# Optimization experiments

Hardware: AMD Instinct MI355X
Metric: run time of the kernel (lower is better)

The kernel has to match this reference:

```python
import jax, jax.numpy as jnp
import numpy as np
import math

D_MODEL = 512
NHEAD = 8
HEAD = D_MODEL // NHEAD


def _pe(length, d):
    pos = np.arange(length)[:, None].astype(np.float32)
    div = np.exp(np.arange(0, d, 2).astype(np.float32) * (-math.log(10000.0) / d))
    pe = np.zeros((length, d), np.float32)
    pe[:, 0::2] = np.sin(pos * div)
    pe[:, 1::2] = np.cos(pos * div)
    return jnp.asarray(pe)


def _ln(x, g, b, eps=1e-5):
    m = x.mean(-1, keepdims=True)
    v = ((x - m) ** 2).mean(-1, keepdims=True)
    return (x - m) / jnp.sqrt(v + eps) * g + b


def _mha(q_in, k_in, v_in, w_in, b_in, w_out, b_out, mask=None):
    d = q_in.shape[-1]
    wq, wk, wv = jnp.split(w_in, 3, axis=0)
    bq, bk, bv = jnp.split(b_in, 3, axis=0)
    B, Sq, _ = q_in.shape
    Sk = k_in.shape[1]
    q = (q_in @ wq.T + bq).reshape(B, Sq, NHEAD, HEAD)
    k = (k_in @ wk.T + bk).reshape(B, Sk, NHEAD, HEAD)
    v = (v_in @ wv.T + bv).reshape(B, Sk, NHEAD, HEAD)
    s = jnp.einsum('bqhd,bkhd->bhqk', q, k) / math.sqrt(HEAD)
    if mask is not None:
        s = s + mask
    a = jax.nn.softmax(s, axis=-1)
    o = jnp.einsum('bhqk,bkhd->bqhd', a, v).reshape(B, Sq, d)
    return o @ w_out.T + b_out


def setup_inputs() -> dict:
    rng = np.random.default_rng(0)
    def r(*s):
        return jnp.asarray(rng.standard_normal(s, dtype=np.float32) * 0.02)
    L, d, ff, di, do = 6, 512, 2048, 64, 64
    B, S, T = 4, 512, 256
    return dict(
        src=jnp.asarray(rng.standard_normal((B, S, di), dtype=np.float32)),
        tgt=jnp.asarray(rng.standard_normal((B, T, do), dtype=np.float32)),
        enc_in_w=r(d, di), enc_in_b=r(d),
        dec_in_w=r(d, do), dec_in_b=r(d),
        out_w=r(do, d), out_b=r(do),
        enc_attn_w=r(L, 3 * d, d), enc_attn_b=r(L, 3 * d),
        enc_out_w=r(L, d, d), enc_out_b=r(L, d),
        enc_ff1_w=r(L, ff, d), enc_ff1_b=r(L, ff),
        enc_ff2_w=r(L, d, ff), enc_ff2_b=r(L, d),
        enc_ln1_g=jnp.ones((L, d)), enc_ln1_b=jnp.zeros((L, d)),
        enc_ln2_g=jnp.ones((L, d)), enc_ln2_b=jnp.zeros((L, d)),
        dec_sa_w=r(L, 3 * d, d), dec_sa_b=r(L, 3 * d),
        dec_sa_out_w=r(L, d, d), dec_sa_out_b=r(L, d),
        dec_ca_w=r(L, 3 * d, d), dec_ca_b=r(L, 3 * d),
        dec_ca_out_w=r(L, d, d), dec_ca_out_b=r(L, d),
        dec_ff1_w=r(L, ff, d), dec_ff1_b=r(L, ff),
        dec_ff2_w=r(L, d, ff), dec_ff2_b=r(L, d),
        dec_ln1_g=jnp.ones((L, d)), dec_ln1_b=jnp.zeros((L, d)),
        dec_ln2_g=jnp.ones((L, d)), dec_ln2_b=jnp.zeros((L, d)),
        dec_ln3_g=jnp.ones((L, d)), dec_ln3_b=jnp.zeros((L, d)),
    )


def reference(src, tgt, enc_in_w, enc_in_b, dec_in_w, dec_in_b, out_w, out_b,
              enc_attn_w, enc_attn_b, enc_out_w, enc_out_b,
              enc_ff1_w, enc_ff1_b, enc_ff2_w, enc_ff2_b,
              enc_ln1_g, enc_ln1_b, enc_ln2_g, enc_ln2_b,
              dec_sa_w, dec_sa_b, dec_sa_out_w, dec_sa_out_b,
              dec_ca_w, dec_ca_b, dec_ca_out_w, dec_ca_out_b,
              dec_ff1_w, dec_ff1_b, dec_ff2_w, dec_ff2_b,
              dec_ln1_g, dec_ln1_b, dec_ln2_g, dec_ln2_b, dec_ln3_g, dec_ln3_b):
    d = D_MODEL
    sq = math.sqrt(d)
    S, T = src.shape[1], tgt.shape[1]
    L = enc_attn_w.shape[0]
    # encoder: 'cosine' pos encoding (dropout disabled / eval)
    x = (src @ enc_in_w.T + enc_in_b) * sq + _pe(S, d)[None]
    for i in range(L):
        a = _mha(x, x, x, enc_attn_w[i], enc_attn_b[i], enc_out_w[i], enc_out_b[i])
        x = _ln(x + a, enc_ln1_g[i], enc_ln1_b[i])
        f = jax.nn.relu(x @ enc_ff1_w[i].T + enc_ff1_b[i]) @ enc_ff2_w[i].T + enc_ff2_b[i]
        x = _ln(x + f, enc_ln2_g[i], enc_ln2_b[i])
    memory = x
    # decoder: teacher-forced prefix loop == single causal-masked pass.
    # NOTE: original adds pe[0] to EVERY step (pos_encoder on a length-1 slice).
    y = (tgt @ dec_in_w.T + dec_in_b) * sq + _pe(1, d)[0]
    mask = jnp.where(jnp.tril(jnp.ones((T, T), bool)), 0.0, -1e9).astype(y.dtype)
    for i in range(L):
        a = _mha(y, y, y, dec_sa_w[i], dec_sa_b[i], dec_sa_out_w[i], dec_sa_out_b[i], mask)
        y = _ln(y + a, dec_ln1_g[i], dec_ln1_b[i])
        c = _mha(y, memory, memory, dec_ca_w[i], dec_ca_b[i], dec_ca_out_w[i], dec_ca_out_b[i])
        y = _ln(y + c, dec_ln2_g[i], dec_ln2_b[i])
        f = jax.nn.relu(y @ dec_ff1_w[i].T + dec_ff1_b[i]) @ dec_ff2_w[i].T + dec_ff2_b[i]
        y = _ln(y + f, dec_ln3_g[i], dec_ln3_b[i])
    return y @ out_w.T + out_b
```

## Files before the change

kernel.cpp:

```cpp
#include <hip/hip_runtime.h>
#include <hip/hip_bf16.h>
#include <math.h>

#define BB 4
#define SEQ 512
#define TGT 256
#define DM 512
#define FFD 2048
#define NH 8
#define HD 64
#define NL 6

typedef unsigned short u16;
typedef __attribute__((ext_vector_type(4))) float f4;
typedef __attribute__((ext_vector_type(4))) unsigned short us4;
typedef __attribute__((ext_vector_type(8))) unsigned short us8;
typedef __attribute__((ext_vector_type(8))) short s8;

__device__ inline u16 f2b(float f) {
    __hip_bfloat16 h = __float2bfloat16(f);
    return *reinterpret_cast<u16*>(&h);
}
__device__ inline float b2f(u16 u) {
    unsigned int x = ((unsigned int)u) << 16;
    float f;
    __builtin_memcpy(&f, &x, 4);
    return f;
}
__device__ inline us4 cvt4(f4 v) {
    us4 u;
    u.x = f2b(v.x); u.y = f2b(v.y); u.z = f2b(v.z); u.w = f2b(v.w);
    return u;
}

struct CastSegs {
    const float* src[24];
    u16* dst[24];
    int cum[25];
    int nseg;
};

__global__ __launch_bounds__(256) void castseg_k(CastSegs cs)
{
    const int g0 = blockIdx.x << 11;
    int s = 0;
    while (g0 >= cs.cum[s + 1]) s++;
    const f4* __restrict__ sp = (const f4*)cs.src[s];
    us4* __restrict__ dp = (us4*)cs.dst[s];
    const int base = g0 - cs.cum[s] + (int)threadIdx.x;

    f4 v[8];
#pragma unroll
    for (int k = 0; k < 8; k++) v[k] = sp[base + (k << 8)];
#pragma unroll
    for (int k = 0; k < 8; k++) dp[base + (k << 8)] = cvt4(v[k]);
}

__global__ void kvbias_k(const float* __restrict__ dec_ca_b, float* __restrict__ out)
{
    int idx = blockIdx.x * blockDim.x + threadIdx.x;
    if (idx >= NL * 2 * DM) return;
    int layer = idx >> 10, j = idx & 1023;
    out[idx] = dec_ca_b[layer * 3 * DM + DM + j];
}

template <int RELU, int OUTF32, int BM, int BN, int PE, int KVMAP>
__global__ __launch_bounds__(256) void mgemm_k(
    const u16* __restrict__ A, const u16* __restrict__ W,
    const float* __restrict__ bias, const u16* __restrict__ resid,
    void* __restrict__ Cv, int M, int N, int K, float alpha)
{
    constexpr int MI = BM / 32;
    constexpr int NJ = BN / 32;
    __shared__ u16 As[2][BM][72];
    __shared__ u16 Bs[2][BN][72];
    const int bm = blockIdx.y * BM, bn = blockIdx.x * BN;
    const int tid = threadIdx.x;
    const int wave = tid >> 6, lane = tid & 63;
    const int wr = (wave >> 1) * (BM / 2), wc = (wave & 1) * (BN / 2);
    const int lm = lane & 15, quad = lane >> 4;
    const int sar = (BM == 64) ? (tid >> 2) : (tid >> 3);
    const int sac = (BM == 64) ? ((tid & 3) * 16) : ((tid & 7) * 8);
    const int sbr = (BN == 64) ? (tid >> 2) : (tid >> 3);
    const int sbc = (BN == 64) ? ((tid & 3) * 16) : ((tid & 7) * 8);

    int brow = bn + sbr;
    if (KVMAP) brow = (brow >> 10) * (3 * DM) + DM + (brow & 1023);

    const u16* Arow = A + (size_t)(bm + sar) * K + sac;
    const u16* Wrow = W + (size_t)brow * K + sbc;

    us8 a0 = *(const us8*)(Arow);
    us8 a1;
    if (BM == 64) a1 = *(const us8*)(Arow + 8);
    us8 b0 = *(const us8*)(Wrow);
    us8 b1;
    if (BN == 64) b1 = *(const us8*)(Wrow + 8);

    f4 acc[MI][NJ];
#pragma unroll
    for (int i = 0; i < MI; i++)
#pragma unroll
        for (int j = 0; j < NJ; j++) acc[i][j] = (f4)(0.f);

    const int nk = K >> 6;
    *(us8*)&As[0][sar][sac] = a0;
    if (BM == 64) *(us8*)&As[0][sar][sac + 8] = a1;
    *(us8*)&Bs[0][sbr][sbc] = b0;
    if (BN == 64) *(us8*)&Bs[0][sbr][sbc + 8] = b1;
    __syncthreads();

    for (int t = 0; t < nk; t++) {
        const int cb = t & 1;
        if (t + 1 < nk) {
            int off = (t + 1) << 6;
            a0 = *(const us8*)(Arow + off);
            if (BM == 64) a1 = *(const us8*)(Arow + off + 8);
            b0 = *(const us8*)(Wrow + off);
            if (BN == 64) b1 = *(const us8*)(Wrow + off + 8);
        }
#pragma unroll
        for (int ks = 0; ks < 2; ks++) {
            s8 af[MI], bfr[NJ];
#pragma unroll
            for (int i = 0; i < MI; i++) af[i] = *(const s8*)&As[cb][wr + i * 16 + lm][ks * 32 + quad * 8];
#pragma unroll
            for (int j = 0; j < NJ; j++) bfr[j] = *(const s8*)&Bs[cb][wc + j * 16 + lm][ks * 32 + quad * 8];
#pragma unroll
            for (int i = 0; i < MI; i++)
#pragma unroll
                for (int j = 0; j < NJ; j++)
                    acc[i][j] = __builtin_amdgcn_mfma_f32_16x16x32_bf16(af[i], bfr[j], acc[i][j], 0, 0, 0);
        }
        if (t + 1 < nk) {
            const int nb = cb ^ 1;
            *(us8*)&As[nb][sar][sac] = a0;
            if (BM == 64) *(us8*)&As[nb][sar][sac + 8] = a1;
            *(us8*)&Bs[nb][sbr][sbc] = b0;
            if (BN == 64) *(us8*)&Bs[nb][sbr][sbc + 8] = b1;
            __syncthreads();
        }
    }

#pragma unroll
    for (int j = 0; j < NJ; j++) {
        int n = bn + wc + j * 16 + lm;
        float bv = bias[n];
        float dv = 0.f;
        if (PE == 1) dv = expf((float)(n & ~1) * (-9.210340371976184f / (float)DM));
#pragma unroll
        for (int i = 0; i < MI; i++) {
#pragma unroll
            for (int r = 0; r < 4; r++) {
                int m = bm + wr + i * 16 + quad * 4 + r;
                float v = (acc[i][j][r] + bv) * alpha;
                if (PE == 1) {
                    float ang = (float)(m & (SEQ - 1)) * dv;
                    v += (n & 1) ? cosf(ang) : sinf(ang);
                }
                if (PE == 2) { if (n & 1) v += 1.f; }
                if (RELU) v = fmaxf(v, 0.f);
                size_t off = (size_t)m * N + n;
                if (resid) v += b2f(resid[off]);
                if (OUTF32) ((float*)Cv)[off] = v;
                else        ((u16*)Cv)[off]  = f2b(v);
            }
        }
    }
}

template <int CAUSAL>
__global__ __launch_bounds__(256) void flash_k(
    const u16* __restrict__ Q, int qs,
    const u16* __restrict__ Kp, int ks,
    const u16* __restrict__ V, int vs,
    u16* __restrict__ O, int Sq, int Sk)
{
    __shared__ u16 Qs[64][72];
    __shared__ u16 Ks[128][72];
    __shared__ u16 Vs[64][136];
    __shared__ u16 Ps[4][16][136];
    const int bm = blockIdx.x * 64;
    const int bh = blockIdx.y, b = bh >> 3, h = bh & 7;
    const int tid = threadIdx.x;
    const int wave = tid >> 6, lane = tid & 63;
    const int lm = lane & 15, quad = lane >> 4;

    const u16* Qb = Q + (size_t)(b * Sq + bm) * qs + h * HD;
    {
        int r = tid >> 2, c = (tid & 3) * 16;
        *(us8*)&Qs[r][c]     = *(const us8*)(Qb + (size_t)r * qs + c);
        *(us8*)&Qs[r][c + 8] = *(const us8*)(Qb + (size_t)r * qs + c + 8);
    }

    float mrow[4], lrow[4];
    f4 o[4];
#pragma unroll
    for (int r = 0; r < 4; r++) { mrow[r] = -1e30f; lrow[r] = 0.f; }
#pragma unroll
    for (int nt = 0; nt < 4; nt++) o[nt] = (f4)(0.f);

    const u16* Kb = Kp + (size_t)(b * Sk) * ks + h * HD;
    const u16* Vb = V + (size_t)(b * Sk) * vs + h * HD;
    int nkt = Sk >> 7;
    if (CAUSAL) { int lim = (bm + 63) / 128 + 1; if (lim < nkt) nkt = lim; }

    const int vd = tid & 63, vkb = tid >> 6;
    const int kr = tid >> 3, kc8 = (tid & 7) * 8;

    for (int kt = 0; kt < nkt; kt++) {
        const u16* Kt = Kb + ((size_t)kt << 7) * ks;
        const u16* Vt = Vb + ((size_t)kt << 7) * vs;
#pragma unroll
        for (int p = 0; p < 4; p++) {
            int r = p * 32 + kr;
            *(us8*)&Ks[r][kc8] = *(const us8*)(Kt + (size_t)r * ks + kc8);
        }
#pragma unroll
        for (int p = 0; p < 32; p++) {
            int kv = p * 4 + vkb;
            Vs[vd][kv] = Vt[(size_t)kv * vs + vd];
        }
        __syncthreads();

        f4 sa[8];
#pragma unroll
        for (int nt = 0; nt < 8; nt++) sa[nt] = (f4)(0.f);
#pragma unroll
        for (int ks2 = 0; ks2 < 2; ks2++) {
            s8 aq = *(const s8*)&Qs[wave * 16 + lm][ks2 * 32 + quad * 8];
#pragma unroll
            for (int nt = 0; nt < 8; nt++) {
                s8 bk = *(const s8*)&Ks[nt * 16 + lm][ks2 * 32 + quad * 8];
                sa[nt] = __builtin_amdgcn_mfma_f32_16x16x32_bf16(aq, bk, sa[nt], 0, 0, 0);
            }
        }
        float tmx[4] = {-1e30f, -1e30f, -1e30f, -1e30f};
#pragma unroll
        for (int nt = 0; nt < 8; nt++) {
#pragma unroll
            for (int r = 0; r < 4; r++) {
                float v = sa[nt][r] * 0.125f;
                if (CAUSAL) {
                    int col = (kt << 7) + nt * 16 + lm;
                    int row = bm + wave * 16 + quad * 4 + r;
                    if (col > row) v = -1e30f;
                }
                sa[nt][r] = v;
                tmx[r] = fmaxf(tmx[r], v);
            }
        }
#pragma unroll
        for (int st = 1; st < 16; st <<= 1)
#pragma unroll
            for (int r = 0; r < 4; r++) tmx[r] = fmaxf(tmx[r], __shfl_xor(tmx[r], st));
        float al[4];
#pragma unroll
        for (int r = 0; r < 4; r++) {
            float mn = fmaxf(mrow[r], tmx[r]);
            al[r] = __expf(mrow[r] - mn);
            mrow[r] = mn;
        }
        float ts[4] = {0.f, 0.f, 0.f, 0.f};
#pragma unroll
        for (int nt = 0; nt < 8; nt++) {
#pragma unroll
            for (int r = 0; r < 4; r++) {
                float pe = __expf(sa[nt][r] - mrow[r]);
                sa[nt][r] = pe;
                ts[r] += pe;
            }
        }
#pragma unroll
        for (int st = 1; st < 16; st <<= 1)
#pragma unroll
            for (int r = 0; r < 4; r++) ts[r] += __shfl_xor(ts[r], st);
#pragma unroll
        for (int r = 0; r < 4; r++) lrow[r] = lrow[r] * al[r] + ts[r];
#pragma unroll
        for (int nt = 0; nt < 4; nt++)
#pragma unroll
            for (int r = 0; r < 4; r++) o[nt][r] *= al[r];
#pragma unroll
        for (int nt = 0; nt < 8; nt++)
#pragma unroll
            for (int r = 0; r < 4; r++)
                Ps[wave][quad * 4 + r][nt * 16 + lm] = f2b(sa[nt][r]);
#pragma unroll
        for (int kc = 0; kc < 4; kc++) {
            s8 ap = *(const s8*)&Ps[wave][lm][kc * 32 + quad * 8];
#pragma unroll
            for (int nt = 0; nt < 4; nt++) {
                s8 bv = *(const s8*)&Vs[nt * 16 + lm][kc * 32 + quad * 8];
                o[nt] = __builtin_amdgcn_mfma_f32_16x16x32_bf16(ap, bv, o[nt], 0, 0, 0);
            }
        }
        __syncthreads();
    }

    float inv[4];
#pragma unroll
    for (int r = 0; r < 4; r++) inv[r] = 1.f / lrow[r];
#pragma unroll
    for (int nt = 0; nt < 4; nt++) {
#pragma unroll
        for (int r = 0; r < 4; r++) {
            int m = bm + wave * 16 + quad * 4 + r;
            O[(size_t)(b * Sq + m) * DM + h * HD + nt * 16 + lm] = f2b(o[nt][r] * inv[r]);
        }
    }
}

__global__ __launch_bounds__(256) void ln_k(u16* __restrict__ x,
                                            const float* __restrict__ g,
                                            const float* __restrict__ b)
{
    const int wave = threadIdx.x >> 6, lane = threadIdx.x & 63;
    const int row = blockIdx.x * 4 + wave;
    u16* xr = x + (size_t)row * DM + lane * 8;
    us8 v8 = *(const us8*)xr;
    float v[8];
    float s = 0.f;
#pragma unroll
    for (int e = 0; e < 8; e++) { v[e] = b2f(v8[e]); s += v[e]; }
#pragma unroll
    for (int st = 1; st < 64; st <<= 1) s += __shfl_xor(s, st);
    float mean = s * (1.f / DM);
    float q = 0.f;
#pragma unroll
    for (int e = 0; e < 8; e++) { float d = v[e] - mean; q += d * d; }
#pragma unroll
    for (int st = 1; st < 64; st <<= 1) q += __shfl_xor(q, st);
    float rstd = rsqrtf(q * (1.f / DM) + 1e-5f);
    f4 g0 = *(const f4*)(g + lane * 8), g1 = *(const f4*)(g + lane * 8 + 4);
    f4 b0 = *(const f4*)(b + lane * 8), b1 = *(const f4*)(b + lane * 8 + 4);
    us8 o;
#pragma unroll
    for (int e = 0; e < 4; e++) {
        o[e]     = f2b((v[e]     - mean) * rstd * g0[e] + b0[e]);
        o[e + 4] = f2b((v[e + 4] - mean) * rstd * g1[e] + b1[e]);
    }
    *(us8*)xr = o;
}

static inline dim3 mg(int M, int N, int BM, int BN) { return dim3(N / BN, M / BM); }

extern "C" void kernel_launch(void* const* d_in, const int* in_sizes, int n_in,
                              void* d_out, int out_size, void* d_ws, size_t ws_size,
                              hipStream_t stream)
{
    const float* src       = (const float*)d_in[0];
    const float* tgt       = (const float*)d_in[1];
    const float* enc_in_w  = (const float*)d_in[2];
    const float* enc_in_b  = (const float*)d_in[3];
    const float* dec_in_w  = (const float*)d_in[4];
    const float* dec_in_b  = (const float*)d_in[5];
    const float* out_w     = (const float*)d_in[6];
    const float* out_b     = (const float*)d_in[7];
    const float* enc_attn_w = (const float*)d_in[8];
    const float* enc_attn_b = (const float*)d_in[9];
    const float* enc_out_w  = (const float*)d_in[10];
    const float* enc_out_b  = (const float*)d_in[11];
    const float* enc_ff1_w  = (const float*)d_in[12];
    const float* enc_ff1_b  = (const float*)d_in[13];
    const float* enc_ff2_w  = (const float*)d_in[14];
    const float* enc_ff2_b  = (const float*)d_in[15];
    const float* enc_ln1_g  = (const float*)d_in[16];
    const float* enc_ln1_b  = (const float*)d_in[17];
    const float* enc_ln2_g  = (const float*)d_in[18];
    const float* enc_ln2_b  = (const float*)d_in[19];
    const float* dec_sa_w     = (const float*)d_in[20];
    const float* dec_sa_b     = (const float*)d_in[21];
    const float* dec_sa_out_w = (const float*)d_in[22];
    const float* dec_sa_out_b = (const float*)d_in[23];
    const float* dec_ca_w     = (const float*)d_in[24];
    const float* dec_ca_b     = (const float*)d_in[25];
    const float* dec_ca_out_w = (const float*)d_in[26];
    const float* dec_ca_out_b = (const float*)d_in[27];
    const float* dec_ff1_w    = (const float*)d_in[28];
    const float* dec_ff1_b    = (const float*)d_in[29];
    const float* dec_ff2_w    = (const float*)d_in[30];
    const float* dec_ff2_b    = (const float*)d_in[31];
    const float* dec_ln1_g    = (const float*)d_in[32];
    const float* dec_ln1_b    = (const float*)d_in[33];
    const float* dec_ln2_g    = (const float*)d_in[34];
    const float* dec_ln2_b    = (const float*)d_in[35];
    const float* dec_ln3_g    = (const float*)d_in[36];
    const float* dec_ln3_b    = (const float*)d_in[37];

    const int ME = BB * SEQ;
    const int MD = BB * TGT;
    const int BH = BB * NH;
    const float SQD = 22.627416997969522f;

    const size_t SZ_ATTN = (size_t)NL * 3 * DM * DM;
    const size_t SZ_OUT  = (size_t)NL * DM * DM;
    const size_t SZ_FF   = (size_t)NL * FFD * DM;

    float* fp = (float*)d_ws;
    float* kvbias = fp; fp += NL * 2 * DM;
    u16* p = (u16*)fp;
    u16* xa   = p; p += (size_t)ME * DM;
    u16* xb   = p; p += (size_t)ME * DM;
    u16* reg1 = p; p += (size_t)ME * FFD;
    u16* tbuf = p; p += (size_t)ME * DM;
    u16* ya   = p; p += (size_t)MD * DM;
    u16* yb   = p; p += (size_t)MD * DM;
    u16* kvall = p; p += (size_t)ME * NL * 2 * DM;
    u16* src_b     = p; p += (size_t)ME * HD;
    u16* tgt_b     = p; p += (size_t)MD * HD;
    u16* enc_in_wb = p; p += (size_t)DM * HD;
    u16* dec_in_wb = p; p += (size_t)DM * HD;
    u16* out_wb    = p; p += (size_t)HD * DM;
    u16* enc_at_wb = p; p += SZ_ATTN;
    u16* enc_ow_wb = p; p += SZ_OUT;
    u16* enc_f1_wb = p; p += SZ_FF;
    u16* enc_f2_wb = p; p += SZ_FF;
    u16* dec_sa_wb = p; p += SZ_ATTN;
    u16* dec_sao_wb = p; p += SZ_OUT;
    u16* dec_ca_wb = p; p += SZ_ATTN;
    u16* dec_cao_wb = p; p += SZ_OUT;
    u16* dec_f1_wb = p; p += SZ_FF;
    u16* dec_f2_wb = p; p += SZ_FF;

    CastSegs cs;
    int ns = 0;
    auto seg = [&](const float* s, u16* d, size_t n) {
        cs.src[ns] = s; cs.dst[ns] = d;
        cs.cum[ns + 1] = cs.cum[ns] + (int)(n / 4);
        ns++;
    };
    cs.cum[0] = 0;
    seg(src,          src_b,     (size_t)ME * HD);
    seg(tgt,          tgt_b,     (size_t)MD * HD);
    seg(enc_in_w,     enc_in_wb, (size_t)DM * HD);
    seg(dec_in_w,     dec_in_wb, (size_t)DM * HD);
    seg(out_w,        out_wb,    (size_t)HD * DM);
    seg(enc_attn_w,   enc_at_wb, SZ_ATTN);
    seg(enc_out_w,    enc_ow_wb, SZ_OUT);
    seg(enc_ff1_w,    enc_f1_wb, SZ_FF);
    seg(enc_ff2_w,    enc_f2_wb, SZ_FF);
    seg(dec_sa_w,     dec_sa_wb, SZ_ATTN);
    seg(dec_sa_out_w, dec_sao_wb, SZ_OUT);
    seg(dec_ca_w,     dec_ca_wb, SZ_ATTN);
    seg(dec_ca_out_w, dec_cao_wb, SZ_OUT);
    seg(dec_ff1_w,    dec_f1_wb, SZ_FF);
    seg(dec_ff2_w,    dec_f2_wb, SZ_FF);
    cs.nseg = ns;
    castseg_k<<<cs.cum[ns] >> 11, 256, 0, stream>>>(cs);
    kvbias_k<<<(NL * 2 * DM + 255) / 256, 256, 0, stream>>>(dec_ca_b, kvbias);

    mgemm_k<0, 0, 64, 32, 1, 0><<<mg(ME, DM, 64, 32), 256, 0, stream>>>(src_b, enc_in_wb, enc_in_b, nullptr, xa, ME, DM, HD, SQD);

    u16* cur = xa; u16* alt = xb;
    for (int i = 0; i < NL; i++) {
        const u16* W = enc_at_wb + (size_t)i * 3 * DM * DM;
        const float* Bw = enc_attn_b + (size_t)i * 3 * DM;
        mgemm_k<0, 0, 64, 64, 0, 0><<<mg(ME, 3 * DM, 64, 64), 256, 0, stream>>>(cur, W, Bw, nullptr, reg1, ME, 3 * DM, DM, 1.f);
        flash_k<0><<<dim3(SEQ / 64, BH), 256, 0, stream>>>(reg1, 3 * DM, reg1 + DM, 3 * DM, reg1 + 2 * DM, 3 * DM, tbuf, SEQ, SEQ);
        mgemm_k<0, 0, 32, 32, 0, 0><<<mg(ME, DM, 32, 32), 256, 0, stream>>>(tbuf, enc_ow_wb + (size_t)i * DM * DM, enc_out_b + (size_t)i * DM, cur, alt, ME, DM, DM, 1.f);
        ln_k<<<ME / 4, 256, 0, stream>>>(alt, enc_ln1_g + (size_t)i * DM, enc_ln1_b + (size_t)i * DM);
        { u16* t = cur; cur = alt; alt = t; }
        mgemm_k<1, 0, 64, 64, 0, 0><<<mg(ME, FFD, 64, 64), 256, 0, stream>>>(cur, enc_f1_wb + (size_t)i * FFD * DM, enc_ff1_b + (size_t)i * FFD, nullptr, reg1, ME, FFD, DM, 1.f);
        mgemm_k<0, 0, 32, 32, 0, 0><<<mg(ME, DM, 32, 32), 256, 0, stream>>>(reg1, enc_f2_wb + (size_t)i * DM * FFD, enc_ff2_b + (size_t)i * DM, cur, alt, ME, DM, FFD, 1.f);
        ln_k<<<ME / 4, 256, 0, stream>>>(alt, enc_ln2_g + (size_t)i * DM, enc_ln2_b + (size_t)i * DM);
        { u16* t = cur; cur = alt; alt = t; }
    }
    u16* mem = cur;

    mgemm_k<0, 0, 64, 64, 0, 1><<<mg(ME, NL * 2 * DM, 64, 64), 256, 0, stream>>>(mem, dec_ca_wb, kvbias, nullptr, kvall, ME, NL * 2 * DM, DM, 1.f);

    mgemm_k<0, 0, 32, 32, 2, 0><<<mg(MD, DM, 32, 32), 256, 0, stream>>>(tgt_b, dec_in_wb, dec_in_b, nullptr, ya, MD, DM, HD, SQD);

    u16* dc = ya; u16* da = yb;
    for (int i = 0; i < NL; i++) {
        const u16* W = dec_sa_wb + (size_t)i * 3 * DM * DM;
        const float* Bw = dec_sa_b + (size_t)i * 3 * DM;
        mgemm_k<0, 0, 64, 32, 0, 0><<<mg(MD, 3 * DM, 64, 32), 256, 0, stream>>>(dc, W, Bw, nullptr, reg1, MD, 3 * DM, DM, 1.f);
        flash_k<1><<<dim3(TGT / 64, BH), 256, 0, stream>>>(reg1, 3 * DM, reg1 + DM, 3 * DM, reg1 + 2 * DM, 3 * DM, tbuf, TGT, TGT);
        mgemm_k<0, 0, 32, 32, 0, 0><<<mg(MD, DM, 32, 32), 256, 0, stream>>>(tbuf, dec_sao_wb + (size_t)i * DM * DM, dec_sa_out_b + (size_t)i * DM, dc, da, MD, DM, DM, 1.f);
        ln_k<<<MD / 4, 256, 0, stream>>>(da, dec_ln1_g + (size_t)i * DM, dec_ln1_b + (size_t)i * DM);
        { u16* t = dc; dc = da; da = t; }

        const u16* Wc = dec_ca_wb + (size_t)i * 3 * DM * DM;
        const float* Bc = dec_ca_b + (size_t)i * 3 * DM;
        u16* qbuf = reg1;
        mgemm_k<0, 0, 32, 32, 0, 0><<<mg(MD, DM, 32, 32), 256, 0, stream>>>(dc, Wc, Bc, nullptr, qbuf, MD, DM, DM, 1.f);
        const u16* kvl = kvall + (size_t)i * 2 * DM;
        flash_k<0><<<dim3(TGT / 64, BH), 256, 0, stream>>>(qbuf, DM, kvl, NL * 2 * DM, kvl + DM, NL * 2 * DM, tbuf, TGT, SEQ);
        mgemm_k<0, 0, 32, 32, 0, 0><<<mg(MD, DM, 32, 32), 256, 0, stream>>>(tbuf, dec_cao_wb + (size_t)i * DM * DM, dec_ca_out_b + (size_t)i * DM, dc, da, MD, DM, DM, 1.f);
        ln_k<<<MD / 4, 256, 0, stream>>>(da, dec_ln2_g + (size_t)i * DM, dec_ln2_b + (size_t)i * DM);
        { u16* t = dc; dc = da; da = t; }

        mgemm_k<1, 0, 64, 32, 0, 0><<<mg(MD, FFD, 64, 32), 256, 0, stream>>>(dc, dec_f1_wb + (size_t)i * FFD * DM, dec_ff1_b + (size_t)i * FFD, nullptr, reg1, MD, FFD, DM, 1.f);
        mgemm_k<0, 0, 32, 32, 0, 0><<<mg(MD, DM, 32, 32), 256, 0, stream>>>(reg1, dec_f2_wb + (size_t)i * DM * FFD, dec_ff2_b + (size_t)i * DM, dc, da, MD, DM, FFD, 1.f);
        ln_k<<<MD / 4, 256, 0, stream>>>(da, dec_ln3_g + (size_t)i * DM, dec_ln3_b + (size_t)i * DM);
        { u16* t = dc; dc = da; da = t; }
    }

    mgemm_k<0, 1, 32, 32, 0, 0><<<mg(MD, HD, 32, 32), 256, 0, stream>>>(dc, out_wb, out_b, nullptr, (float*)d_out, MD, HD, DM, 1.f);
}
```

Baseline: 1.211 ms.

## Fuse LayerNorm into GEMM epilogues and prologues via atomic row statistics

Removes the standalone LayerNorm kernels. GEMMs that produce a residual sum now accumulate per-row sum and sum-of-squares with atomics into a zeroed stats buffer. Consumer GEMMs normalize the A operand while staging it into shared memory and normalize the residual in their epilogue. This cuts 30 kernel launches and their global read/write passes. The cost is extra atomics and per-element normalize math in the GEMMs. Variance computed as E[x²]−mean² in fp32 is less numerically robust than the two-pass version.

```diff
diff --git a/kernel.cpp b/kernel.cpp
--- a/kernel.cpp
+++ b/kernel.cpp
@@ -33,6 +33,21 @@
     return u;
 }
 
+__device__ inline us8 lnx8(us8 y, float mean, float rstd,
+                           const float* __restrict__ g, const float* __restrict__ b) {
+    us8 o;
+#pragma unroll
+    for (int e = 0; e < 8; e++)
+        o[e] = f2b((b2f(y[e]) - mean) * rstd * g[e] + b[e]);
+    return o;
+}
+
+__global__ __launch_bounds__(256) void zero_k(float* __restrict__ p, int n)
+{
+    int i = blockIdx.x * 256 + threadIdx.x;
+    if (i < n) p[i] = 0.f;
+}
+
 struct CastSegs {
     const float* src[24];
     u16* dst[24];
@@ -64,11 +79,15 @@
     out[idx] = dec_ca_b[layer * 3 * DM + DM + j];
 }
 
-template <int RELU, int OUTF32, int BM, int BN, int PE, int KVMAP>
+template <int RELU, int OUTF32, int BM, int BN, int PE, int KVMAP,
+          int LNA, int LNRES, int LNOUT>
 __global__ __launch_bounds__(256) void mgemm_k(
     const u16* __restrict__ A, const u16* __restrict__ W,
     const float* __restrict__ bias, const u16* __restrict__ resid,
-    void* __restrict__ Cv, int M, int N, int K, float alpha)
+    void* __restrict__ Cv,
+    const float* __restrict__ lnst_in, const float* __restrict__ g_in,
+    const float* __restrict__ b_in, float* __restrict__ lnst_out,
+    int M, int N, int K, float alpha)
 {
     constexpr int MI = BM / 32;
     constexpr int NJ = BN / 32;
@@ -90,6 +109,14 @@
     const u16* Arow = A + (size_t)(bm + sar) * K + sac;
     const u16* Wrow = W + (size_t)brow * K + sbc;
 
+    float meanA = 0.f, rstdA = 0.f;
+    if (LNA) {
+        int rowA = bm + sar;
+        float s = lnst_in[rowA * 2], q = lnst_in[rowA * 2 + 1];
+        meanA = s * (1.f / DM);
+        rstdA = rsqrtf(q * (1.f / DM) - meanA * meanA + 1e-5f);
+    }
+
     us8 a0 = *(const us8*)(Arow);
     us8 a1;
     if (BM == 64) a1 = *(const us8*)(Arow + 8);
@@ -104,16 +131,22 @@
         for (int j = 0; j < NJ; j++) acc[i][j] = (f4)(0.f);
 
     const int nk = K >> 6;
-    *(us8*)&As[0][sar][sac] = a0;
-    if (BM == 64) *(us8*)&As[0][sar][sac + 8] = a1;
+    if (LNA) {
+        *(us8*)&As[0][sar][sac] = lnx8(a0, meanA, rstdA, g_in + sac, b_in + sac);
+        if (BM == 64) *(us8*)&As[0][sar][sac + 8] = lnx8(a1, meanA, rstdA, g_in + sac + 8, b_in + sac + 8);
+    } else {
+        *(us8*)&As[0][sar][sac] = a0;
+        if (BM == 64) *(us8*)&As[0][sar][sac + 8] = a1;
+    }
     *(us8*)&Bs[0][sbr][sbc] = b0;
     if (BN == 64) *(us8*)&Bs[0][sbr][sbc + 8] = b1;
     __syncthreads();
 
     for (int t = 0; t < nk; t++) {
         const int cb = t & 1;
+        int off = 0;
         if (t + 1 < nk) {
-            int off = (t + 1) << 6;
+            off = (t + 1) << 6;
             a0 = *(const us8*)(Arow + off);
             if (BM == 64) a1 = *(const us8*)(Arow + off + 8);
             b0 = *(const us8*)(Wrow + off);
@@ -134,18 +167,46 @@
         }
         if (t + 1 < nk) {
             const int nb = cb ^ 1;
-            *(us8*)&As[nb][sar][sac] = a0;
-            if (BM == 64) *(us8*)&As[nb][sar][sac + 8] = a1;
+            if (LNA) {
+                *(us8*)&As[nb][sar][sac] = lnx8(a0, meanA, rstdA, g_in + off + sac, b_in + off + sac);
+                if (BM == 64) *(us8*)&As[nb][sar][sac + 8] = lnx8(a1, meanA, rstdA, g_in + off + sac + 8, b_in + off + sac + 8);
+            } else {
+                *(us8*)&As[nb][sar][sac] = a0;
+                if (BM == 64) *(us8*)&As[nb][sar][sac + 8] = a1;
+            }
             *(us8*)&Bs[nb][sbr][sbc] = b0;
             if (BN == 64) *(us8*)&Bs[nb][sbr][sbc + 8] = b1;
             __syncthreads();
         }
     }
 
+    float meanR[MI][4], rstdR[MI][4];
+    if (LNRES) {
+#pragma unroll
+        for (int i = 0; i < MI; i++)
+#pragma unroll
+            for (int r = 0; r < 4; r++) {
+                int m = bm + wr + i * 16 + quad * 4 + r;
+                float s = lnst_in[m * 2], q = lnst_in[m * 2 + 1];
+                float mn = s * (1.f / DM);
+                meanR[i][r] = mn;
+                rstdR[i][r] = rsqrtf(q * (1.f / DM) - mn * mn + 1e-5f);
+            }
+    }
+    float so[MI][4], qo[MI][4];
+    if (LNOUT) {
+#pragma unroll
+        for (int i = 0; i < MI; i++)
+#pragma unroll
+            for (int r = 0; r < 4; r++) { so[i][r] = 0.f; qo[i][r] = 0.f; }
+    }
+
 #pragma unroll
     for (int j = 0; j < NJ; j++) {
         int n = bn + wc + j * 16 + lm;
         float bv = bias[n];
+        float gR = 0.f, bRv = 0.f;
+        if (LNRES) { gR = g_in[n]; bRv = b_in[n]; }
         float dv = 0.f;
         if (PE == 1) dv = expf((float)(n & ~1) * (-9.210340371976184f / (float)DM));
 #pragma unroll
@@ -161,10 +222,37 @@
                 if (PE == 2) { if (n & 1) v += 1.f; }
                 if (RELU) v = fmaxf(v, 0.f);
                 size_t off = (size_t)m * N + n;
-                if (resid) v += b2f(resid[off]);
+                if (resid) {
+                    float rv = b2f(resid[off]);
+                    if (LNRES) rv = (rv - meanR[i][r]) * rstdR[i][r] * gR + bRv;
+                    v += rv;
+                }
                 if (OUTF32) ((float*)Cv)[off] = v;
                 else        ((u16*)Cv)[off]  = f2b(v);
+                if (LNOUT) { so[i][r] += v; qo[i][r] += v * v; }
             }
+        }
+    }
+
+    if (LNOUT) {
+#pragma unroll
+        for (int st = 1; st < 16; st <<= 1)
+#pragma unroll
+            for (int i = 0; i < MI; i++)
+#pragma unroll
+                for (int r = 0; r < 4; r++) {
+                    so[i][r] += __shfl_xor(so[i][r], st);
+                    qo[i][r] += __shfl_xor(qo[i][r], st);
+                }
+        if (lm == 0) {
+#pragma unroll
+            for (int i = 0; i < MI; i++)
+#pragma unroll
+                for (int r = 0; r < 4; r++) {
+                    int m = bm + wr + i * 16 + quad * 4 + r;
+                    atomicAdd(&lnst_out[m * 2],     so[i][r]);
+                    atomicAdd(&lnst_out[m * 2 + 1], qo[i][r]);
+                }
         }
     }
 }
@@ -309,38 +397,6 @@
             O[(size_t)(b * Sq + m) * DM + h * HD + nt * 16 + lm] = f2b(o[nt][r] * inv[r]);
         }
     }
-}
-
-__global__ __launch_bounds__(256) void ln_k(u16* __restrict__ x,
-                                            const float* __restrict__ g,
-                                            const float* __restrict__ b)
-{
-    const int wave = threadIdx.x >> 6, lane = threadIdx.x & 63;
-    const int row = blockIdx.x * 4 + wave;
-    u16* xr = x + (size_t)row * DM + lane * 8;
-    us8 v8 = *(const us8*)xr;
-    float v[8];
-    float s = 0.f;
-#pragma unroll
-    for (int e = 0; e < 8; e++) { v[e] = b2f(v8[e]); s += v[e]; }
-#pragma unroll
-    for (int st = 1; st < 64; st <<= 1) s += __shfl_xor(s, st);
-    float mean = s * (1.f / DM);
-    float q = 0.f;
-#pragma unroll
-    for (int e = 0; e < 8; e++) { float d = v[e] - mean; q += d * d; }
-#pragma unroll
-    for (int st = 1; st < 64; st <<= 1) q += __shfl_xor(q, st);
-    float rstd = rsqrtf(q * (1.f / DM) + 1e-5f);
-    f4 g0 = *(const f4*)(g + lane * 8), g1 = *(const f4*)(g + lane * 8 + 4);
-    f4 b0 = *(const f4*)(b + lane * 8), b1 = *(const f4*)(b + lane * 8 + 4);
-    us8 o;
-#pragma unroll
-    for (int e = 0; e < 4; e++) {
-        o[e]     = f2b((v[e]     - mean) * rstd * g0[e] + b0[e]);
-        o[e + 4] = f2b((v[e + 4] - mean) * rstd * g1[e] + b1[e]);
-    }
-    *(us8*)xr = o;
 }
 
 static inline dim3 mg(int M, int N, int BM, int BN) { return dim3(N / BN, M / BM); }
@@ -398,6 +454,8 @@
     const size_t SZ_FF   = (size_t)NL * FFD * DM;
 
     float* fp = (float*)d_ws;
+    const int ENC_ST = 12 * 2048 * 2, DEC_ST = 18 * 1024 * 2;
+    float* stats = fp; fp += ENC_ST + DEC_ST;
     float* kvbias = fp; fp += NL * 2 * DM;
     u16* p = (u16*)fp;
     u16* xa   = p; p += (size_t)ME * DM;
@@ -422,6 +480,11 @@
     u16* dec_cao_wb = p; p += SZ_OUT;
     u16* dec_f1_wb = p; p += SZ_FF;
     u16* dec_f2_wb = p; p += SZ_FF;
+
+    auto eSt = [&](int i, int s) { return stats + (size_t)(i * 2 + s) * 2048 * 2; };
+    auto dSt = [&](int i, int s) { return stats + ENC_ST + (size_t)(i * 3 + s) * 1024 * 2; };
+
+    zero_k<<<(ENC_ST + DEC_ST + 255) / 256, 256, 0, stream>>>(stats, ENC_ST + DEC_ST);
 
     CastSegs cs;
     int ns = 0;
@@ -450,53 +513,94 @@
     castseg_k<<<cs.cum[ns] >> 11, 256, 0, stream>>>(cs);
     kvbias_k<<<(NL * 2 * DM + 255) / 256, 256, 0, stream>>>(dec_ca_b, kvbias);
 
-    mgemm_k<0, 0, 64, 32, 1, 0><<<mg(ME, DM, 64, 32), 256, 0, stream>>>(src_b, enc_in_wb, enc_in_b, nullptr, xa, ME, DM, HD, SQD);
+    mgemm_k<0, 0, 64, 32, 1, 0, 0, 0, 0><<<mg(ME, DM, 64, 32), 256, 0, stream>>>(
+        src_b, enc_in_wb, enc_in_b, nullptr, xa, nullptr, nullptr, nullptr, nullptr, ME, DM, HD, SQD);
 
     u16* cur = xa; u16* alt = xb;
     for (int i = 0; i < NL; i++) {
         const u16* W = enc_at_wb + (size_t)i * 3 * DM * DM;
         const float* Bw = enc_attn_b + (size_t)i * 3 * DM;
-        mgemm_k<0, 0, 64, 64, 0, 0><<<mg(ME, 3 * DM, 64, 64), 256, 0, stream>>>(cur, W, Bw, nullptr, reg1, ME, 3 * DM, DM, 1.f);
+        const float* pSt = (i > 0) ? eSt(i - 1, 1) : nullptr;
+        const float* pG  = enc_ln2_g + (size_t)(i - 1) * DM;
+        const float* pB  = enc_ln2_b + (size_t)(i - 1) * DM;
+        if (i == 0)
+            mgemm_k<0, 0, 64, 64, 0, 0, 0, 0, 0><<<mg(ME, 3 * DM, 64, 64), 256, 0, stream>>>(
+                cur, W, Bw, nullptr, reg1, nullptr, nullptr, nullptr, nullptr, ME, 3 * DM, DM, 1.f);
+        else
+            mgemm_k<0, 0, 64, 64, 0, 0, 1, 0, 0><<<mg(ME, 3 * DM, 64, 64), 256, 0, stream>>>(
+                cur, W, Bw, nullptr, reg1, pSt, pG, pB, nullptr, ME, 3 * DM, DM, 1.f);
         flash_k<0><<<dim3(SEQ / 64, BH), 256, 0, stream>>>(reg1, 3 * DM, reg1 + DM, 3 * DM, reg1 + 2 * DM, 3 * DM, tbuf, SEQ, SEQ);
-        mgemm_k<0, 0, 32, 32, 0, 0><<<mg(ME, DM, 32, 32), 256, 0, stream>>>(tbuf, enc_ow_wb + (size_t)i * DM * DM, enc_out_b + (size_t)i * DM, cur, alt, ME, DM, DM, 1.f);
-        ln_k<<<ME / 4, 256, 0, stream>>>(alt, enc_ln1_g + (size_t)i * DM, enc_ln1_b + (size_t)i * DM);
+        if (i == 0)
+            mgemm_k<0, 0, 32, 32, 0, 0, 0, 0, 1><<<mg(ME, DM, 32, 32), 256, 0, stream>>>(
+                tbuf, enc_ow_wb + (size_t)i * DM * DM, enc_out_b + (size_t)i * DM, cur, alt,
+                nullptr, nullptr, nullptr, eSt(i, 0), ME, DM, DM, 1.f);
+        else
+            mgemm_k<0, 0, 32, 32, 0, 0, 0, 1, 1><<<mg(ME, DM, 32, 32), 256, 0, stream>>>(
+                tbuf, enc_ow_wb + (size_t)i * DM * DM, enc_out_b + (size_t)i * DM, cur, alt,
+                pSt, pG, pB, eSt(i, 0), ME, DM, DM, 1.f);
         { u16* t = cur; cur = alt; alt = t; }
-        mgemm_k<1, 0, 64, 64, 0, 0><<<mg(ME, FFD, 64, 64), 256, 0, stream>>>(cur, enc_f1_wb + (size_t)i * FFD * DM, enc_ff1_b + (size_t)i * FFD, nullptr, reg1, ME, FFD, DM, 1.f);
-        mgemm_k<0, 0, 32, 32, 0, 0><<<mg(ME, DM, 32, 32), 256, 0, stream>>>(reg1, enc_f2_wb + (size_t)i * DM * FFD, enc_ff2_b + (size_t)i * DM, cur, alt, ME, DM, FFD, 1.f);
-        ln_k<<<ME / 4, 256, 0, stream>>>(alt, enc_ln2_g + (size_t)i * DM, enc_ln2_b + (size_t)i * DM);
+        mgemm_k<1, 0, 64, 64, 0, 0, 1, 0, 0><<<mg(ME, FFD, 64, 64), 256, 0, stream>>>(
+            cur, enc_f1_wb + (size_t)i * FFD * DM, enc_ff1_b + (size_t)i * FFD, nullptr, reg1,
+            eSt(i, 0), enc_ln1_g + (size_t)i * DM, enc_ln1_b + (size_t)i * DM, nullptr, ME, FFD, DM, 1.f);
+        mgemm_k<0, 0, 32, 32, 0, 0, 0, 1, 1><<<mg(ME, DM, 32, 32), 256, 0, stream>>>(
+            reg1, enc_f2_wb + (size_t)i * DM * FFD, enc_ff2_b + (size_t)i * DM, cur, alt,
+            eSt(i, 0), enc_ln1_g + (size_t)i * DM, enc_ln1_b + (size_t)i * DM, eSt(i, 1), ME, DM, FFD, 1.f);
         { u16* t = cur; cur = alt; alt = t; }
     }
     u16* mem = cur;
 
-    mgemm_k<0, 0, 64, 64, 0, 1><<<mg(ME, NL * 2 * DM, 64, 64), 256, 0, stream>>>(mem, dec_ca_wb, kvbias, nullptr, kvall, ME, NL * 2 * DM, DM, 1.f);
-
-    mgemm_k<0, 0, 32, 32, 2, 0><<<mg(MD, DM, 32, 32), 256, 0, stream>>>(tgt_b, dec_in_wb, dec_in_b, nullptr, ya, MD, DM, HD, SQD);
+    mgemm_k<0, 0, 64, 64, 0, 1, 1, 0, 0><<<mg(ME, NL * 2 * DM, 64, 64), 256, 0, stream>>>(
+        mem, dec_ca_wb, kvbias, nullptr, kvall,
+        eSt(5, 1), enc_ln2_g + (size_t)5 * DM, enc_ln2_b + (size_t)5 * DM, nullptr, ME, NL * 2 * DM, DM, 1.f);
+
+    mgemm_k<0, 0, 32, 32, 2, 0, 0, 0, 0><<<mg(MD, DM, 32, 32), 256, 0, stream>>>(
+        tgt_b, dec_in_wb, dec_in_b, nullptr, ya, nullptr, nullptr, nullptr, nullptr, MD, DM, HD, SQD);
 
     u16* dc = ya; u16* da = yb;
     for (int i = 0; i < NL; i++) {
         const u16* W = dec_sa_wb + (size_t)i * 3 * DM * DM;
         const float* Bw = dec_sa_b + (size_t)i * 3 * DM;
-        mgemm_k<0, 0, 64, 32, 0, 0><<<mg(MD, 3 * DM, 64, 32), 256, 0, stream>>>(dc, W, Bw, nullptr, reg1, MD, 3 * DM, DM, 1.f);
+        const float* pSt = (i > 0) ? dSt(i - 1, 2) : nullptr;
+        const float* pG  = dec_ln3_g + (size_t)(i - 1) * DM;
+        const float* pB  = dec_ln3_b + (size_t)(i - 1) * DM;
+        if (i == 0)
+            mgemm_k<0, 0, 64, 32, 0, 0, 0, 0, 0><<<mg(MD, 3 * DM, 64, 32), 256, 0, stream>>>(
+                dc, W, Bw, nullptr, reg1, nullptr, nullptr, nullptr, nullptr, MD, 3 * DM, DM, 1.f);
+        else
+            mgemm_k<0, 0, 64, 32, 0, 0, 1, 0, 0><<<mg(MD, 3 * DM, 64, 32), 256, 0, stream>>>(
+                dc, W, Bw, nullptr, reg1, pSt, pG, pB, nullptr, MD, 3 * DM, DM, 1.f);
         flash_k<1><<<dim3(TGT / 64, BH), 256, 0, stream>>>(reg1, 3 * DM, reg1 + DM, 3 * DM, reg1 + 2 * DM, 3 * DM, tbuf, TGT, TGT);
-        mgemm_k<0, 0, 32, 32, 0, 0><<<mg(MD, DM, 32, 32), 256, 0, stream>>>(tbuf, dec_sao_wb + (size_t)i * DM * DM, dec_sa_out_b + (size_t)i * DM, dc, da, MD, DM, DM, 1.f);
-        ln_k<<<MD / 4, 256, 0, stream>>>(da, dec_ln1_g + (size_t)i * DM, dec_ln1_b + (size_t)i * DM);
+        if (i == 0)
+            mgemm_k<0, 0, 32, 32, 0, 0, 0, 0, 1><<<mg(MD, DM, 32, 32), 256, 0, stream>>>(
+                tbuf, dec_sao_wb + (size_t)i * DM * DM, dec_sa_out_b + (size_t)i * DM, dc, da,
+                nullptr, nullptr, nullptr, dSt(i, 0), MD, DM, DM, 1.f);
+        else
+            mgemm_k<0, 0, 32, 32, 0, 0, 0, 1, 1><<<mg(MD, DM, 32, 32), 256, 0, stream>>>(
+                tbuf, dec_sao_wb + (size_t)i * DM * DM, dec_sa_out_b + (size_t)i * DM, dc, da,
+                pSt, pG, pB, dSt(i, 0), MD, DM, DM, 1.f);
         { u16* t = dc; dc = da; da = t; }
 
-        const u16* Wc = dec_ca_wb + (size_t)i * 3 * DM * DM;
-        const float* Bc = dec_ca_b + (size_t)i * 3 * DM;
         u16* qbuf = reg1;
-        mgemm_k<0, 0, 32, 32, 0, 0><<<mg(MD, DM, 32, 32), 256, 0, stream>>>(dc, Wc, Bc, nullptr, qbuf, MD, DM, DM, 1.f);
+        mgemm_k<0, 0, 32, 32, 0, 0, 1, 0, 0><<<mg(MD, DM, 32, 32), 256, 0, stream>>>(
+            dc, dec_ca_wb + (size_t)i * 3 * DM * DM, dec_ca_b + (size_t)i * 3 * DM, nullptr, qbuf,
+            dSt(i, 0), dec_ln1_g + (size_t)i * DM, dec_ln1_b + (size_t)i * DM, nullptr, MD, DM, DM, 1.f);
         const u16* kvl = kvall + (size_t)i * 2 * DM;
         flash_k<0><<<dim3(TGT / 64, BH), 256, 0, stream>>>(qbuf, DM, kvl, NL * 2 * DM, kvl + DM, NL * 2 * DM, tbuf, TGT, SEQ);
-        mgemm_k<0, 0, 32, 32, 0, 0><<<mg(MD, DM, 32, 32), 256, 0, stream>>>(tbuf, dec_cao_wb + (size_t)i * DM * DM, dec_ca_out_b + (size_t)i * DM, dc, da, MD, DM, DM, 1.f);
-        ln_k<<<MD / 4, 256, 0, stream>>>(da, dec_ln2_g + (size_t)i * DM, dec_ln2_b + (size_t)i * DM);
+        mgemm_k<0, 0, 32, 32, 0, 0, 0, 1, 1><<<mg(MD, DM, 32, 32), 256, 0, stream>>>(
+            tbuf, dec_cao_wb + (size_t)i * DM * DM, dec_ca_out_b + (size_t)i * DM, dc, da,
+            dSt(i, 0), dec_ln1_g + (size_t)i * DM, dec_ln1_b + (size_t)i * DM, dSt(i, 1), MD, DM, DM, 1.f);
         { u16* t = dc; dc = da; da = t; }
 
-        mgemm_k<1, 0, 64, 32, 0, 0><<<mg(MD, FFD, 64, 32), 256, 0, stream>>>(dc, dec_f1_wb + (size_t)i * FFD * DM, dec_ff1_b + (size_t)i * FFD, nullptr, reg1, MD, FFD, DM, 1.f);
-        mgemm_k<0, 0, 32, 32, 0, 0><<<mg(MD, DM, 32, 32), 256, 0, stream>>>(reg1, dec_f2_wb + (size_t)i * DM * FFD, dec_ff2_b + (size_t)i * DM, dc, da, MD, DM, FFD, 1.f);
-        ln_k<<<MD / 4, 256, 0, stream>>>(da, dec_ln3_g + (size_t)i * DM, dec_ln3_b + (size_t)i * DM);
+        mgemm_k<1, 0, 64, 32, 0, 0, 1, 0, 0><<<mg(MD, FFD, 64, 32), 256, 0, stream>>>(
+            dc, dec_f1_wb + (size_t)i * FFD * DM, dec_ff1_b + (size_t)i * FFD, nullptr, reg1,
+            dSt(i, 1), dec_ln2_g + (size_t)i * DM, dec_ln2_b + (size_t)i * DM, nullptr, MD, FFD, DM, 1.f);
+        mgemm_k<0, 0, 32, 32, 0, 0, 0, 1, 1><<<mg(MD, DM, 32, 32), 256, 0, stream>>>(
+            reg1, dec_f2_wb + (size_t)i * DM * FFD, dec_ff2_b + (size_t)i * DM, dc, da,
+            dSt(i, 1), dec_ln2_g + (size_t)i * DM, dec_ln2_b + (size_t)i * DM, dSt(i, 2), MD, DM, FFD, 1.f);
         { u16* t = dc; dc = da; da = t; }
     }
 
-    mgemm_k<0, 1, 32, 32, 0, 0><<<mg(MD, HD, 32, 32), 256, 0, stream>>>(dc, out_wb, out_b, nullptr, (float*)d_out, MD, HD, DM, 1.f);
-}
+    mgemm_k<0, 1, 32, 32, 0, 0, 1, 0, 0><<<mg(MD, HD, 32, 32), 256, 0, stream>>>(
+        dc, out_wb, out_b, nullptr, (float*)d_out,
+        dSt(5, 2), dec_ln3_g + (size_t)5 * DM, dec_ln3_b + (size_t)5 * DM, nullptr, MD, HD, DM, 1.f);
+}
```

Result: slower. 1.670 ms (+37.9%).
